# Optimization experiments

Measured on AMD Instinct MI355X. Metric: run time of the kernel, lower is better.

The kernel has to match this reference:

```python
import jax, jax.numpy as jnp
import numpy as np

N, S, A0, NPTS, L, P = 4096, 128, 5, 11, 256, 64
A = A0 + NPTS          # atoms per residue after pseudo-points
RBF_BINS = 16
RBF_MIN, RBF_MAX = 0.0, 12.0
EPS = 1e-6


def _normalize(v, axis=-1):
    return v / jnp.sqrt(jnp.sum(v * v, axis=axis, keepdims=True) + EPS)


def _extract_frames(pos):
    # pos: [N, A0, 3]; atoms 0=N, 1=CA, 2=C. Gram-Schmidt rigid frame.
    n, ca, c = pos[:, 0], pos[:, 1], pos[:, 2]
    e1 = _normalize(c - ca)
    v2 = n - ca
    u2 = v2 - e1 * jnp.sum(e1 * v2, axis=-1, keepdims=True)
    e2 = _normalize(u2)
    e3 = jnp.cross(e1, e2)
    rot = jnp.stack([e1, e2, e3], axis=-1)  # [N,3,3], columns are axes
    return rot, ca


def _distance_rbf(d):
    centers = jnp.linspace(RBF_MIN, RBF_MAX, RBF_BINS)      # [16]
    sigma = (RBF_MAX - RBF_MIN) / RBF_BINS
    z = (d[..., None] - centers) / sigma
    return jnp.exp(-z * z)


def _forward(local, pos, smol_type, smol_pos, smol_mask,
             w_points, w_type, w_local, w_dir, w_dist,
             ln_scale, ln_offset, w_mlp1, b_mlp1, w_mlp2, b_mlp2,
             w_gate, w_out):
    rot, trans = _extract_frames(pos)
    # LinearToPoints: local-frame points -> global frame
    p_local = (local @ w_points).reshape(N, NPTS, 3)
    pseudo = jnp.einsum('nij,nkj->nki', rot, p_local) + trans[:, None]
    pos_all = jnp.concatenate([pos, pseudo], axis=-2)        # [N, A, 3]

    rel = smol_pos[:, :, None, :] - pos_all[:, None, :, :]   # [N, S, A, 3]
    dist = jnp.sqrt(jnp.sum(rel * rel, axis=-1) + EPS)       # [N, S, A]
    directions = (rel / dist[..., None]).reshape(N, S, A * 3)
    distances = _distance_rbf(dist).reshape(N, S, A * RBF_BINS)

    pair = jax.nn.one_hot(smol_type, 7, dtype=local.dtype) @ w_type
    pair = pair + (local @ w_local)[:, None]
    pair = pair + directions @ w_dir
    pair = pair + distances @ w_dist                          # [N, S, P]

    mu = jnp.mean(pair, axis=-1, keepdims=True)
    var = jnp.mean((pair - mu) ** 2, axis=-1, keepdims=True)
    pair = (pair - mu) * jax.lax.rsqrt(var + 1e-5) * ln_scale + ln_offset

    pair = jax.nn.gelu(pair @ w_mlp1 + b_mlp1) @ w_mlp2 + b_mlp2

    m = smol_mask[..., None].astype(pair.dtype)
    pair = jnp.sum(pair * m, axis=1) / jnp.maximum(jnp.sum(m, axis=1), 1.0)

    gate = local @ w_gate
    pair = jax.nn.gelu(gate) * pair
    return pair @ w_out                                       # [N, L]


def setup_inputs() -> dict:
    key = jax.random.key(0)
    ks = jax.random.split(key, 16)
    sc = lambda k, sh: (jax.random.normal(k, sh, jnp.float32)
                        / np.sqrt(sh[0]).astype(np.float32))
    inp = {}
    inp['local'] = jax.random.normal(ks[0], (N, L), jnp.float32)
    inp['pos'] = jax.random.normal(ks[1], (N, A0, 3), jnp.float32) * 3.0
    inp['smol_type'] = jax.random.randint(ks[2], (N, S), 0, 7)
    inp['smol_pos'] = jax.random.normal(ks[3], (N, S, 3), jnp.float32) * 3.0
    inp['smol_mask'] = jax.random.randint(ks[4], (N, S), 0, 2).astype(bool)
    inp['w_points'] = sc(ks[5], (L, NPTS * 3))
    inp['w_type'] = sc(ks[6], (7, P))
    inp['w_local'] = sc(ks[7], (L, P))
    inp['w_dir'] = sc(ks[8], (A * 3, P))
    inp['w_dist'] = sc(ks[9], (A * RBF_BINS, P))
    inp['ln_scale'] = jnp.ones((P,), jnp.float32)
    inp['ln_offset'] = jnp.zeros((P,), jnp.float32)
    inp['w_mlp1'] = sc(ks[10], (P, 2 * P))
    inp['b_mlp1'] = jnp.zeros((2 * P,), jnp.float32)
    inp['w_mlp2'] = sc(ks[11], (2 * P, P))
    inp['b_mlp2'] = jnp.zeros((P,), jnp.float32)
    inp['w_gate'] = sc(ks[12], (L, P))
    inp['w_out'] = sc(ks[13], (P, L)) * 0.02
    return inp


def reference(local, pos, smol_type, smol_pos, smol_mask,
              w_points, w_type, w_local, w_dir, w_dist,
              ln_scale, ln_offset, w_mlp1, b_mlp1, w_mlp2, b_mlp2,
              w_gate, w_out):
    return _forward(local, pos, smol_type, smol_pos, smol_mask,
                    w_points, w_type, w_local, w_dir, w_dist,
                    ln_scale, ln_offset, w_mlp1, b_mlp1, w_mlp2, b_mlp2,
                    w_gate, w_out)
```

## Files before the change

### kernel.cpp

```cpp
#include <hip/hip_runtime.h>
#include <math.h>

#define NRES 4096
#define SS   128
#define A0C  5
#define ATOT 16
#define LD   256
#define PD   64
#define HD   128

typedef __attribute__((ext_vector_type(8))) short bf16x8;
typedef __attribute__((ext_vector_type(4))) float f32x4;
typedef __attribute__((ext_vector_type(4))) unsigned int u32x4;

__device__ __forceinline__ unsigned short f2bf(float x){
    unsigned int u = __builtin_bit_cast(unsigned int, x);
    unsigned int r = u + 0x7FFFu + ((u >> 16) & 1u);
    return (unsigned short)(r >> 16);
}
__device__ __forceinline__ unsigned short f2bfhu(float x){
    return (unsigned short)((__builtin_bit_cast(unsigned int, x) + 0x8000u) >> 16);
}
__device__ __forceinline__ unsigned int pk2bf(float lo, float hi){
    unsigned int a = __builtin_bit_cast(unsigned int, lo) + 0x8000u;
    unsigned int b = __builtin_bit_cast(unsigned int, hi) + 0x8000u;
    return __builtin_amdgcn_perm(b, a, 0x07060302u);
}
__device__ __forceinline__ float gelu_f(float x){
    float e = __builtin_amdgcn_exp2f(-2.3022082f * x * (1.0f + 0.044715f * x * x));
    return x * __builtin_amdgcn_rcpf(1.0f + e);
}
__device__ __forceinline__ f32x4 MFMA(bf16x8 a, bf16x8 b, f32x4 c){
    return __builtin_amdgcn_mfma_f32_16x16x32_bf16(a, b, c, 0, 0, 0);
}

__global__ void smol_prep(const float* __restrict__ wdist, const float* __restrict__ wdir,
                          const float* __restrict__ wm1,  const float* __restrict__ wm2,
                          unsigned short* __restrict__ ws)
{
    int i = blockIdx.x * 256 + threadIdx.x;
    if (i < 16384){
        int nn = i >> 8, k = i & 255;
        ws[i] = f2bf(wdist[k*64 + nn]);
    } else if (i < 20480){
        int j = i - 16384; int nn = j >> 6, k = j & 63;
        ws[i] = (k < 48) ? f2bf(wdir[k*64 + nn]) : (unsigned short)0;
    } else if (i < 28672){
        int j = i - 20480; int nn = j >> 6, k = j & 63;
        ws[i] = f2bf(wm1[k*128 + nn]);
    } else if (i < 36864){
        int j = i - 28672; int nn = j >> 7, k = j & 127;
        ws[i] = f2bf(wm2[k*64 + nn]);
    }
}

struct __align__(16) SMem {
    unsigned short wbuf[64*72];
    union {
        float  dist[128*17];
        unsigned short hidT[128*72];
    };
    unsigned short pairT[128*72];
    float  loc[LD];
    float  posall3[ATOT*3];
    float  pl[33];
    float  rot[9];
    float  ca3[3];
    float  wtypef[7*PD];
    float  basev[PD];
    float  gatevv[PD];
    float  lnsc[PD], lnof[PD];
    float  b1v[HD], b2v[PD];
    int    typef[SS];
    float  maskf[SS];
    float  red[4*PD];
    float  fin[PD];
    float  cnt;
};

__device__ __forceinline__ float dirv2(const SMem& sm, float px, float py, float pz,
                                       int sl, int k){
    int kc = (k < 48) ? k : 47;
    int a = (kc * 21846) >> 16;
    int c = kc - 3*a;
    float pc = (c == 0) ? px : ((c == 1) ? py : pz);
    float e = (pc - sm.posall3[a*3+c]) * __builtin_amdgcn_rcpf(sm.dist[sl*17 + a]);
    return (k < 48) ? e : 0.0f;
}

__device__ __forceinline__ void loadStage(const unsigned short* __restrict__ src, int stride,
                                          int tid, u32x4& a, u32x4& b){
    int r = tid >> 3, s = (tid & 7) * 8;
    a = *(const u32x4*)&src[r*stride + s];
    b = *(const u32x4*)&src[(r+32)*stride + s];
}
__device__ __forceinline__ void pubStage(u32x4 a, u32x4 b, unsigned short* dst, int tid){
    __syncthreads();
    int r = tid >> 3, s = (tid & 7) * 8;
    *(u32x4*)&dst[r*72 + s]      = a;
    *(u32x4*)&dst[(r+32)*72 + s] = b;
    __syncthreads();
}

#define RBF_FRAG(av, sl) do {                                               \
    float dA_ = sm.dist[(sl)*17 + 2*kk + (g>>1)] * 1.60149654f;             \
    float z0_ = dA_ - (b0c + 0.00000000f);                                  \
    float z1_ = dA_ - (b0c + 1.28119724f);                                  \
    float z2_ = dA_ - (b0c + 2.56239447f);                                  \
    float z3_ = dA_ - (b0c + 3.84359171f);                                  \
    float z4_ = dA_ - (b0c + 5.12478894f);                                  \
    float z5_ = dA_ - (b0c + 6.40598618f);                                  \
    float z6_ = dA_ - (b0c + 7.68718342f);                                  \
    float z7_ = dA_ - (b0c + 8.96838065f);                                  \
    unsigned int w0_ = pk2bf(__builtin_amdgcn_exp2f((-z0_)*z0_),            \
                             __builtin_amdgcn_exp2f((-z1_)*z1_));           \
    unsigned int w1_ = pk2bf(__builtin_amdgcn_exp2f((-z2_)*z2_),            \
                             __builtin_amdgcn_exp2f((-z3_)*z3_));           \
    unsigned int w2_ = pk2bf(__builtin_amdgcn_exp2f((-z4_)*z4_),            \
                             __builtin_amdgcn_exp2f((-z5_)*z5_));           \
    unsigned int w3_ = pk2bf(__builtin_amdgcn_exp2f((-z6_)*z6_),            \
                             __builtin_amdgcn_exp2f((-z7_)*z7_));           \
    av = __builtin_bit_cast(bf16x8, (u32x4){w0_, w1_, w2_, w3_});           \
} while(0)

__global__ __launch_bounds__(256, 3)
void smol_fused(const float* __restrict__ g_local,
                const float* __restrict__ g_pos,
                const int*   __restrict__ g_type,
                const float* __restrict__ g_spos,
                const int*   __restrict__ g_mask,
                const float* __restrict__ w_points,
                const float* __restrict__ w_local,
                const float* __restrict__ w_type,
                const float* __restrict__ ln_scale,
                const float* __restrict__ ln_offset,
                const float* __restrict__ b_mlp1,
                const float* __restrict__ b_mlp2,
                const float* __restrict__ w_gate,
                const float* __restrict__ w_out,
                const unsigned short* __restrict__ ws,
                float* __restrict__ g_out)
{
    __shared__ SMem sm;
    const int n    = blockIdx.x;
    const int tid  = threadIdx.x;
    const int wv   = tid >> 6;
    const int lane = tid & 63;
    const int cB   = lane & 15;
    const int g    = lane >> 4;
    const int sl0  = 32*wv + cB;
    const int sl1  = sl0 + 16;

    const unsigned short* wsD   = ws;
    const unsigned short* wsDir = ws + 16384;
    const unsigned short* wsM1  = ws + 20480;
    const unsigned short* wsM2  = ws + 28672;

    sm.loc[tid] = g_local[n*LD + tid];
    sm.wtypef[tid] = w_type[tid];
    if (tid < 7*PD - 256) sm.wtypef[256 + tid] = w_type[256 + tid];
    if (tid < PD){ sm.lnsc[tid] = ln_scale[tid]; sm.lnof[tid] = ln_offset[tid]; sm.b2v[tid] = b_mlp2[tid]; }
    if (tid < HD) sm.b1v[tid] = b_mlp1[tid];
    if (tid < SS){ sm.typef[tid] = g_type[n*SS + tid];
                   sm.maskf[tid] = (g_mask[n*SS + tid] != 0) ? 1.0f : 0.0f; }
    if (tid >= 128 && tid < 128 + A0C*3) sm.posall3[tid-128] = g_pos[n*A0C*3 + (tid-128)];
    __syncthreads();

    if (tid < 33){
        float a = 0.f;
        for (int i = 0; i < LD; ++i) a += sm.loc[i] * w_points[i*33 + tid];
        sm.pl[tid] = a;
    } else if (tid >= 64 && tid < 128){
        int p = tid - 64; float a = 0.f;
        for (int i = 0; i < LD; ++i) a += sm.loc[i] * w_local[i*PD + p];
        sm.basev[p] = a;
    } else if (tid >= 128 && tid < 192){
        int p = tid - 128; float a = 0.f;
        for (int i = 0; i < LD; ++i) a += sm.loc[i] * w_gate[i*PD + p];
        sm.gatevv[p] = gelu_f(a);
    } else if (tid == 255){
        float nx=sm.posall3[0], ny=sm.posall3[1], nz=sm.posall3[2];
        float cax=sm.posall3[3], cay=sm.posall3[4], caz=sm.posall3[5];
        float cx=sm.posall3[6], cy=sm.posall3[7], cz=sm.posall3[8];
        float v1x=cx-cax, v1y=cy-cay, v1z=cz-caz;
        float r = 1.0f/sqrtf(v1x*v1x + v1y*v1y + v1z*v1z + 1e-6f);
        float e1x=v1x*r, e1y=v1y*r, e1z=v1z*r;
        float v2x=nx-cax, v2y=ny-cay, v2z=nz-caz;
        float dp = e1x*v2x + e1y*v2y + e1z*v2z;
        float u2x=v2x-e1x*dp, u2y=v2y-e1y*dp, u2z=v2z-e1z*dp;
        r = 1.0f/sqrtf(u2x*u2x + u2y*u2y + u2z*u2z + 1e-6f);
        float e2x=u2x*r, e2y=u2y*r, e2z=u2z*r;
        float e3x=e1y*e2z-e1z*e2y, e3y=e1z*e2x-e1x*e2z, e3z=e1x*e2y-e1y*e2x;
        sm.rot[0]=e1x; sm.rot[1]=e2x; sm.rot[2]=e3x;
        sm.rot[3]=e1y; sm.rot[4]=e2y; sm.rot[5]=e3y;
        sm.rot[6]=e1z; sm.rot[7]=e2z; sm.rot[8]=e3z;
        sm.ca3[0]=cax; sm.ca3[1]=cay; sm.ca3[2]=caz;
    } else if (tid == 254){
        float c = 0.f;
        for (int s = 0; s < SS; ++s) c += sm.maskf[s];
        sm.cnt = c;
    }
    __syncthreads();
    if (tid < 33){
        int k = tid / 3, i2 = tid - k*3;
        sm.posall3[(A0C + k)*3 + i2] =
            sm.rot[i2*3+0]*sm.pl[k*3+0] + sm.rot[i2*3+1]*sm.pl[k*3+1] +
            sm.rot[i2*3+2]*sm.pl[k*3+2] + sm.ca3[i2];
    }
    __syncthreads();

    const float px0 = g_spos[(n*SS + sl0)*3 + 0];
    const float py0 = g_spos[(n*SS + sl0)*3 + 1];
    const float pz0 = g_spos[(n*SS + sl0)*3 + 2];
    const float px1 = g_spos[(n*SS + sl1)*3 + 0];
    const float py1 = g_spos[(n*SS + sl1)*3 + 1];
    const float pz1 = g_spos[(n*SS + sl1)*3 + 2];

    u32x4 pfa, pfb;
    loadStage(wsD, 256, tid, pfa, pfb);

    #pragma unroll
    for (int aa = 0; aa < 4; ++aa){
        int a = g*4 + aa;
        float ax = sm.posall3[a*3+0], ay = sm.posall3[a*3+1], az = sm.posall3[a*3+2];
        float rx0 = px0-ax, ry0 = py0-ay, rz0 = pz0-az;
        sm.dist[sl0*17 + a] = sqrtf(rx0*rx0 + ry0*ry0 + rz0*rz0 + 1e-6f);
        float rx1 = px1-ax, ry1 = py1-ay, rz1 = pz1-az;
        sm.dist[sl1*17 + a] = sqrtf(rx1*rx1 + ry1*ry1 + rz1*rz1 + 1e-6f);
    }

    const float lnS0 = sm.lnsc[cB+ 0], lnS1 = sm.lnsc[cB+16],
                lnS2 = sm.lnsc[cB+32], lnS3 = sm.lnsc[cB+48];
    const float lnO0 = sm.lnof[cB+ 0], lnO1 = sm.lnof[cB+16],
                lnO2 = sm.lnof[cB+32], lnO3 = sm.lnof[cB+48];
    const float bs0 = sm.basev[cB+ 0], bs1 = sm.basev[cB+16],
                bs2 = sm.basev[cB+32], bs3 = sm.basev[cB+48];
    const float b1a0 = sm.b1v[cB+0*16], b1a1 = sm.b1v[cB+1*16],
                b1a2 = sm.b1v[cB+2*16], b1a3 = sm.b1v[cB+3*16];
    const float b1b0 = sm.b1v[cB+4*16], b1b1 = sm.b1v[cB+5*16],
                b1b2 = sm.b1v[cB+6*16], b1b3 = sm.b1v[cB+7*16];

    const float b0c = (float)((g&1) * 8) * 1.28119724f;

    f32x4 accP0 = {0.f,0.f,0.f,0.f}, accP1 = accP0, accP2 = accP0, accP3 = accP0;
    f32x4 accQ0 = accP0, accQ1 = accP0, accQ2 = accP0, accQ3 = accP0;

    for (int h = 0; h < 4; ++h){
        pubStage(pfa, pfb, sm.wbuf, tid);
        if (h < 3) loadStage(wsD + (h+1)*64, 256, tid, pfa, pfb);
        else       loadStage(wsDir, 64, tid, pfa, pfb);
        #pragma unroll
        for (int kkl = 0; kkl < 2; ++kkl){
            const int kk = h*2 + kkl;
            bf16x8 av0, av1;
            RBF_FRAG(av0, sl0);
            RBF_FRAG(av1, sl1);
            const unsigned short* bb = &sm.wbuf[cB*72 + kkl*32 + g*8];
            bf16x8 B0 = *(const bf16x8*)(bb +  0*72);
            bf16x8 B1 = *(const bf16x8*)(bb + 16*72);
            bf16x8 B2 = *(const bf16x8*)(bb + 32*72);
            bf16x8 B3 = *(const bf16x8*)(bb + 48*72);
            accP0 = MFMA(av0, B0, accP0);  accQ0 = MFMA(av1, B0, accQ0);
            accP1 = MFMA(av0, B1, accP1);  accQ1 = MFMA(av1, B1, accQ1);
            accP2 = MFMA(av0, B2, accP2);  accQ2 = MFMA(av1, B2, accQ2);
            accP3 = MFMA(av0, B3, accP3);  accQ3 = MFMA(av1, B3, accQ3);
        }
    }

    pubStage(pfa, pfb, sm.wbuf, tid);
    loadStage(wsM1, 64, tid, pfa, pfb);
    #pragma unroll
    for (int kk = 0; kk < 2; ++kk){
        int k0 = kk*32 + g*8;
        unsigned int a0w0 = pk2bf(dirv2(sm,px0,py0,pz0,sl0,k0+0), dirv2(sm,px0,py0,pz0,sl0,k0+1));
        unsigned int a0w1 = pk2bf(dirv2(sm,px0,py0,pz0,sl0,k0+2), dirv2(sm,px0,py0,pz0,sl0,k0+3));
        unsigned int a0w2 = pk2bf(dirv2(sm,px0,py0,pz0,sl0,k0+4), dirv2(sm,px0,py0,pz0,sl0,k0+5));
        unsigned int a0w3 = pk2bf(dirv2(sm,px0,py0,pz0,sl0,k0+6), dirv2(sm,px0,py0,pz0,sl0,k0+7));
        bf16x8 av0 = __builtin_bit_cast(bf16x8, (u32x4){a0w0,a0w1,a0w2,a0w3});
        unsigned int a1w0 = pk2bf(dirv2(sm,px1,py1,pz1,sl1,k0+0), dirv2(sm,px1,py1,pz1,sl1,k0+1));
        unsigned int a1w1 = pk2bf(dirv2(sm,px1,py1,pz1,sl1,k0+2), dirv2(sm,px1,py1,pz1,sl1,k0+3));
        unsigned int a1w2 = pk2bf(dirv2(sm,px1,py1,pz1,sl1,k0+4), dirv2(sm,px1,py1,pz1,sl1,k0+5));
        unsigned int a1w3 = pk2bf(dirv2(sm,px1,py1,pz1,sl1,k0+6), dirv2(sm,px1,py1,pz1,sl1,k0+7));
        bf16x8 av1 = __builtin_bit_cast(bf16x8, (u32x4){a1w0,a1w1,a1w2,a1w3});
        const unsigned short* bb = &sm.wbuf[cB*72 + k0];
        bf16x8 B0 = *(const bf16x8*)(bb +  0*72);
        bf16x8 B1 = *(const bf16x8*)(bb + 16*72);
        bf16x8 B2 = *(const bf16x8*)(bb + 32*72);
        bf16x8 B3 = *(const bf16x8*)(bb + 48*72);
        accP0 = MFMA(av0, B0, accP0);  accQ0 = MFMA(av1, B0, accQ0);
        accP1 = MFMA(av0, B1, accP1);  accQ1 = MFMA(av1, B1, accQ1);
        accP2 = MFMA(av0, B2, accP2);  accQ2 = MFMA(av1, B2, accQ2);
        accP3 = MFMA(av0, B3, accP3);  accQ3 = MFMA(av1, B3, accQ3);
    }

    #pragma unroll
    for (int t = 0; t < 2; ++t){
        #pragma unroll
        for (int r = 0; r < 4; ++r){
            int slr = 32*wv + 16*t + g*4 + r;
            int ty  = sm.typef[slr];
            float a0 = (t==0 ? accP0[r] : accQ0[r]);
            float a1 = (t==0 ? accP1[r] : accQ1[r]);
            float a2 = (t==0 ? accP2[r] : accQ2[r]);
            float a3 = (t==0 ? accP3[r] : accQ3[r]);
            float v0 = a0 + bs0 + sm.wtypef[ty*PD + cB +  0];
            float v1 = a1 + bs1 + sm.wtypef[ty*PD + cB + 16];
            float v2 = a2 + bs2 + sm.wtypef[ty*PD + cB + 32];
            float v3 = a3 + bs3 + sm.wtypef[ty*PD + cB + 48];
            float ssum = v0+v1+v2+v3;
            ssum += __shfl_xor(ssum,1); ssum += __shfl_xor(ssum,2);
            ssum += __shfl_xor(ssum,4); ssum += __shfl_xor(ssum,8);
            float mu = ssum * (1.0f/64.0f);
            float d0=v0-mu, d1=v1-mu, d2=v2-mu, d3=v3-mu;
            float sq = d0*d0+d1*d1+d2*d2+d3*d3;
            sq += __shfl_xor(sq,1); sq += __shfl_xor(sq,2);
            sq += __shfl_xor(sq,4); sq += __shfl_xor(sq,8);
            float inv = __builtin_amdgcn_rsqf(sq*(1.0f/64.0f) + 1e-5f);
            unsigned short* pr = &sm.pairT[slr*72];
            pr[cB +  0] = f2bfhu(d0*inv*lnS0 + lnO0);
            pr[cB + 16] = f2bfhu(d1*inv*lnS1 + lnO1);
            pr[cB + 32] = f2bfhu(d2*inv*lnS2 + lnO2);
            pr[cB + 48] = f2bfhu(d3*inv*lnS3 + lnO3);
        }
    }

    f32x4 accO0 = {0.f,0.f,0.f,0.f}, accO1 = accO0, accO2 = accO0, accO3 = accO0;
    f32x4 accN0 = accO0, accN1 = accO0, accN2 = accO0, accN3 = accO0;

    f32x4 accH0 = {0.f,0.f,0.f,0.f}, accH1 = accH0, accH2 = accH0, accH3 = accH0;
    f32x4 accI0 = accH0, accI1 = accH0, accI2 = accH0, accI3 = accH0;
    pubStage(pfa, pfb, sm.wbuf, tid);
    loadStage(wsM2, 128, tid, pfa, pfb);
    #pragma unroll
    for (int kk = 0; kk < 2; ++kk){
        bf16x8 a0 = *(const bf16x8*)&sm.pairT[sl0*72 + kk*32 + g*8];
        bf16x8 a1 = *(const bf16x8*)&sm.pairT[sl1*72 + kk*32 + g*8];
        const unsigned short* bb = &sm.wbuf[cB*72 + kk*32 + g*8];
        bf16x8 B0 = *(const bf16x8*)(bb + 0*16*72);
        bf16x8 B1 = *(const bf16x8*)(bb + 1*16*72);
        bf16x8 B2 = *(const bf16x8*)(bb + 2*16*72);
        bf16x8 B3 = *(const bf16x8*)(bb + 3*16*72);
        accH0 = MFMA(a0, B0, accH0);  accI0 = MFMA(a1, B0, accI0);
        accH1 = MFMA(a0, B1, accH1);  accI1 = MFMA(a1, B1, accI1);
        accH2 = MFMA(a0, B2, accH2);  accI2 = MFMA(a1, B2, accI2);
        accH3 = MFMA(a0, B3, accH3);  accI3 = MFMA(a1, B3, accI3);
    }
    #pragma unroll
    for (int r = 0; r < 4; ++r){
        int slr0 = 32*wv + g*4 + r;
        unsigned short* hr0 = &sm.hidT[slr0*72];
        hr0[cB + 0*16] = f2bfhu(gelu_f(accH0[r] + b1a0));
        hr0[cB + 1*16] = f2bfhu(gelu_f(accH1[r] + b1a1));
        hr0[cB + 2*16] = f2bfhu(gelu_f(accH2[r] + b1a2));
        hr0[cB + 3*16] = f2bfhu(gelu_f(accH3[r] + b1a3));
        unsigned short* hr1 = &sm.hidT[(slr0+16)*72];
        hr1[cB + 0*16] = f2bfhu(gelu_f(accI0[r] + b1a0));
        hr1[cB + 1*16] = f2bfhu(gelu_f(accI1[r] + b1a1));
        hr1[cB + 2*16] = f2bfhu(gelu_f(accI2[r] + b1a2));
        hr1[cB + 3*16] = f2bfhu(gelu_f(accI3[r] + b1a3));
    }

    pubStage(pfa, pfb, sm.wbuf, tid);
    loadStage(wsM1 + 64*64, 64, tid, pfa, pfb);
    #pragma unroll
    for (int kkl = 0; kkl < 2; ++kkl){
        bf16x8 a0 = *(const bf16x8*)&sm.hidT[sl0*72 + kkl*32 + g*8];
        bf16x8 a1 = *(const bf16x8*)&sm.hidT[sl1*72 + kkl*32 + g*8];
        const unsigned short* bb = &sm.wbuf[cB*72 + kkl*32 + g*8];
        bf16x8 B0 = *(const bf16x8*)(bb + 0*16*72);
        bf16x8 B1 = *(const bf16x8*)(bb + 1*16*72);
        bf16x8 B2 = *(const bf16x8*)(bb + 2*16*72);
        bf16x8 B3 = *(const bf16x8*)(bb + 3*16*72);
        accO0 = MFMA(a0, B0, accO0);  accN0 = MFMA(a1, B0, accN0);
        accO1 = MFMA(a0, B1, accO1);  accN1 = MFMA(a1, B1, accN1);
        accO2 = MFMA(a0, B2, accO2);  accN2 = MFMA(a1, B2, accN2);
        accO3 = MFMA(a0, B3, accO3);  accN3 = MFMA(a1, B3, accN3);
    }

    f32x4 accH4 = {0.f,0.f,0.f,0.f}, accH5 = accH4, accH6 = accH4, accH7 = accH4;
    f32x4 accI4 = accH4, accI5 = accH4, accI6 = accH4, accI7 = accH4;
    pubStage(pfa, pfb, sm.wbuf, tid);
    loadStage(wsM2 + 64, 128, tid, pfa, pfb);
    #pragma unroll
    for (int kk = 0; kk < 2; ++kk){
        bf16x8 a0 = *(const bf16x8*)&sm.pairT[sl0*72 + kk*32 + g*8];
        bf16x8 a1 = *(const bf16x8*)&sm.pairT[sl1*72 + kk*32 + g*8];
        const unsigned short* bb = &sm.wbuf[cB*72 + kk*32 + g*8];
        bf16x8 B0 = *(const bf16x8*)(bb + 0*16*72);
        bf16x8 B1 = *(const bf16x8*)(bb + 1*16*72);
        bf16x8 B2 = *(const bf16x8*)(bb + 2*16*72);
        bf16x8 B3 = *(const bf16x8*)(bb + 3*16*72);
        accH4 = MFMA(a0, B0, accH4);  accI4 = MFMA(a1, B0, accI4);
        accH5 = MFMA(a0, B1, accH5);  accI5 = MFMA(a1, B1, accI5);
        accH6 = MFMA(a0, B2, accH6);  accI6 = MFMA(a1, B2, accI6);
        accH7 = MFMA(a0, B3, accH7);  accI7 = MFMA(a1, B3, accI7);
    }
    #pragma unroll
    for (int r = 0; r < 4; ++r){
        int slr0 = 32*wv + g*4 + r;
        unsigned short* hr0 = &sm.hidT[slr0*72];
        hr0[cB + 0*16] = f2bfhu(gelu_f(accH4[r] + b1b0));
        hr0[cB + 1*16] = f2bfhu(gelu_f(accH5[r] + b1b1));
        hr0[cB + 2*16] = f2bfhu(gelu_f(accH6[r] + b1b2));
        hr0[cB + 3*16] = f2bfhu(gelu_f(accH7[r] + b1b3));
        unsigned short* hr1 = &sm.hidT[(slr0+16)*72];
        hr1[cB + 0*16] = f2bfhu(gelu_f(accI4[r] + b1b0));
        hr1[cB + 1*16] = f2bfhu(gelu_f(accI5[r] + b1b1));
        hr1[cB + 2*16] = f2bfhu(gelu_f(accI6[r] + b1b2));
        hr1[cB + 3*16] = f2bfhu(gelu_f(accI7[r] + b1b3));
    }

    pubStage(pfa, pfb, sm.wbuf, tid);
    #pragma unroll
    for (int kkl = 0; kkl < 2; ++kkl){
        bf16x8 a0 = *(const bf16x8*)&sm.hidT[sl0*72 + kkl*32 + g*8];
        bf16x8 a1 = *(const bf16x8*)&sm.hidT[sl1*72 + kkl*32 + g*8];
        const unsigned short* bb = &sm.wbuf[cB*72 + kkl*32 + g*8];
        bf16x8 B0 = *(const bf16x8*)(bb + 0*16*72);
        bf16x8 B1 = *(const bf16x8*)(bb + 1*16*72);
        bf16x8 B2 = *(const bf16x8*)(bb + 2*16*72);
        bf16x8 B3 = *(const bf16x8*)(bb + 3*16*72);
        accO0 = MFMA(a0, B0, accO0);  accN0 = MFMA(a1, B0, accN0);
        accO1 = MFMA(a0, B1, accO1);  accN1 = MFMA(a1, B1, accN1);
        accO2 = MFMA(a0, B2, accO2);  accN2 = MFMA(a1, B2, accN2);
        accO3 = MFMA(a0, B3, accO3);  accN3 = MFMA(a1, B3, accN3);
    }

    float pooled0 = 0.f, pooled1 = 0.f, pooled2 = 0.f, pooled3 = 0.f;
    #pragma unroll
    for (int r = 0; r < 4; ++r){
        float m0f = sm.maskf[32*wv + g*4 + r];
        float m1f = sm.maskf[32*wv + 16 + g*4 + r];
        pooled0 += m0f * accO0[r] + m1f * accN0[r];
        pooled1 += m0f * accO1[r] + m1f * accN1[r];
        pooled2 += m0f * accO2[r] + m1f * accN2[r];
        pooled3 += m0f * accO3[r] + m1f * accN3[r];
    }

    pooled0 += __shfl_xor(pooled0,16); pooled0 += __shfl_xor(pooled0,32);
    pooled1 += __shfl_xor(pooled1,16); pooled1 += __shfl_xor(pooled1,32);
    pooled2 += __shfl_xor(pooled2,16); pooled2 += __shfl_xor(pooled2,32);
    pooled3 += __shfl_xor(pooled3,16); pooled3 += __shfl_xor(pooled3,32);
    if (g == 0){
        sm.red[wv*PD + cB +  0] = pooled0;
        sm.red[wv*PD + cB + 16] = pooled1;
        sm.red[wv*PD + cB + 32] = pooled2;
        sm.red[wv*PD + cB + 48] = pooled3;
    }
    __syncthreads();
    if (tid < PD){
        float v = sm.red[tid] + sm.red[PD + tid] + sm.red[2*PD + tid] + sm.red[3*PD + tid];
        float mc = fmaxf(sm.cnt, 1.0f);
        v = (v + sm.cnt * sm.b2v[tid]) / mc;
        sm.fin[tid] = sm.gatevv[tid] * v;
    }
    __syncthreads();
    {
        float a = 0.f;
        #pragma unroll 4
        for (int p = 0; p < PD; ++p) a += sm.fin[p] * w_out[p*LD + tid];
        g_out[n*LD + tid] = a;
    }
}

extern "C" void kernel_launch(void* const* d_in, const int* in_sizes, int n_in,
                              void* d_out, int out_size, void* d_ws, size_t ws_size,
                              hipStream_t stream)
{
    (void)in_sizes; (void)n_in; (void)out_size; (void)ws_size;
    const float* g_local   = (const float*)d_in[0];
    const float* g_pos     = (const float*)d_in[1];
    const int*   g_type    = (const int*)  d_in[2];
    const float* g_spos    = (const float*)d_in[3];
    const int*   g_mask    = (const int*)  d_in[4];
    const float* w_points  = (const float*)d_in[5];
    const float* w_type    = (const float*)d_in[6];
    const float* w_local   = (const float*)d_in[7];
    const float* w_dir     = (const float*)d_in[8];
    const float* w_dist    = (const float*)d_in[9];
    const float* ln_scale  = (const float*)d_in[10];
    const float* ln_offset = (const float*)d_in[11];
    const float* w_mlp1    = (const float*)d_in[12];
    const float* b_mlp1    = (const float*)d_in[13];
    const float* w_mlp2    = (const float*)d_in[14];
    const float* b_mlp2    = (const float*)d_in[15];
    const float* w_gate    = (const float*)d_in[16];
    const float* w_out     = (const float*)d_in[17];

    unsigned short* ws = (unsigned short*)d_ws;

    smol_prep<<<dim3(144), dim3(256), 0, stream>>>(w_dist, w_dir, w_mlp1, w_mlp2, ws);

    smol_fused<<<dim3(NRES), dim3(256), 0, stream>>>(
        g_local, g_pos, g_type, g_spos, g_mask,
        w_points, w_local, w_type, ln_scale, ln_offset,
        b_mlp1, b_mlp2, w_gate, w_out, ws, (float*)d_out);
}
```

Before: 132.6 us.

## Keep layer-normed pair tile in registers via transposed MFMA and shuffles

Measured after the change: 122.3 us. -7.8%, faster.

```diff
diff --git a/kernel.cpp b/kernel.cpp
--- a/kernel.cpp
+++ b/kernel.cpp
@@ -60,21 +60,21 @@
         float  dist[128*17];
         unsigned short hidT[128*72];
     };
-    unsigned short pairT[128*72];
     float  loc[LD];
     float  posall3[ATOT*3];
+    float  wtypef[7*PD];
+    float  basev[PD];
+    float  lnsc[PD], lnof[PD];
+    float  b1v[HD];
+    float  b2v[PD];
+    float  gatevv[PD];
+    float  maskf[SS];
+    float  red[4*PD];
+    float  fin[PD];
+    int    typef[SS];
     float  pl[33];
     float  rot[9];
     float  ca3[3];
-    float  wtypef[7*PD];
-    float  basev[PD];
-    float  gatevv[PD];
-    float  lnsc[PD], lnof[PD];
-    float  b1v[HD], b2v[PD];
-    int    typef[SS];
-    float  maskf[SS];
-    float  red[4*PD];
-    float  fin[PD];
     float  cnt;
 };
 
@@ -123,7 +123,44 @@
     av = __builtin_bit_cast(bf16x8, (u32x4){w0_, w1_, w2_, w3_});           \
 } while(0)
 
-__global__ __launch_bounds__(256, 3)
+#define MK_FRAG(F, Lm0, Lm1) do {                                           \
+    float a0_ = __shfl(Lm0[0], srcA), b0_ = __shfl(Lm1[0], srcA);           \
+    float a1_ = __shfl(Lm0[1], srcA), b1_ = __shfl(Lm1[1], srcA);           \
+    float a2_ = __shfl(Lm0[2], srcA), b2_ = __shfl(Lm1[2], srcA);           \
+    float a3_ = __shfl(Lm0[3], srcA), b3_ = __shfl(Lm1[3], srcA);           \
+    float a4_ = __shfl(Lm0[0], srcB), b4_ = __shfl(Lm1[0], srcB);           \
+    float a5_ = __shfl(Lm0[1], srcB), b5_ = __shfl(Lm1[1], srcB);           \
+    float a6_ = __shfl(Lm0[2], srcB), b6_ = __shfl(Lm1[2], srcB);           \
+    float a7_ = __shfl(Lm0[3], srcB), b7_ = __shfl(Lm1[3], srcB);           \
+    float v0_ = hi ? b0_ : a0_;  float v1_ = hi ? b1_ : a1_;                \
+    float v2_ = hi ? b2_ : a2_;  float v3_ = hi ? b3_ : a3_;                \
+    float v4_ = hi ? b4_ : a4_;  float v5_ = hi ? b5_ : a5_;                \
+    float v6_ = hi ? b6_ : a6_;  float v7_ = hi ? b7_ : a7_;                \
+    F = __builtin_bit_cast(bf16x8, (u32x4){pk2bf(v0_,v1_), pk2bf(v2_,v3_),  \
+                                           pk2bf(v4_,v5_), pk2bf(v6_,v7_)});\
+} while(0)
+
+#define TILE_LN(L0, L1, L2, L3, A0, A1, A2, A3, tyv) do {                   \
+    f32x4 v0_ = A0 + bV0 + *(const f32x4*)&sm.wtypef[(tyv)*PD + pb +  0];   \
+    f32x4 v1_ = A1 + bV1 + *(const f32x4*)&sm.wtypef[(tyv)*PD + pb + 16];   \
+    f32x4 v2_ = A2 + bV2 + *(const f32x4*)&sm.wtypef[(tyv)*PD + pb + 32];   \
+    f32x4 v3_ = A3 + bV3 + *(const f32x4*)&sm.wtypef[(tyv)*PD + pb + 48];   \
+    float ss_ = v0_[0]+v0_[1]+v0_[2]+v0_[3] + v1_[0]+v1_[1]+v1_[2]+v1_[3]   \
+              + v2_[0]+v2_[1]+v2_[2]+v2_[3] + v3_[0]+v3_[1]+v3_[2]+v3_[3];  \
+    ss_ += __shfl_xor(ss_,16); ss_ += __shfl_xor(ss_,32);                   \
+    float mu_ = ss_ * (1.0f/64.0f);                                         \
+    f32x4 d0_ = v0_ - mu_, d1_ = v1_ - mu_, d2_ = v2_ - mu_, d3_ = v3_ - mu_;\
+    float sq_ = d0_[0]*d0_[0]+d0_[1]*d0_[1]+d0_[2]*d0_[2]+d0_[3]*d0_[3]     \
+              + d1_[0]*d1_[0]+d1_[1]*d1_[1]+d1_[2]*d1_[2]+d1_[3]*d1_[3]     \
+              + d2_[0]*d2_[0]+d2_[1]*d2_[1]+d2_[2]*d2_[2]+d2_[3]*d2_[3]     \
+              + d3_[0]*d3_[0]+d3_[1]*d3_[1]+d3_[2]*d3_[2]+d3_[3]*d3_[3];    \
+    sq_ += __shfl_xor(sq_,16); sq_ += __shfl_xor(sq_,32);                   \
+    float inv_ = __builtin_amdgcn_rsqf(sq_*(1.0f/64.0f) + 1e-5f);           \
+    L0 = d0_*inv_*sV0 + oV0;  L1 = d1_*inv_*sV1 + oV1;                      \
+    L2 = d2_*inv_*sV2 + oV2;  L3 = d3_*inv_*sV3 + oV3;                      \
+} while(0)
+
+__global__ __launch_bounds__(256, 4)
 void smol_fused(const float* __restrict__ g_local,
                 const float* __restrict__ g_pos,
                 const int*   __restrict__ g_type,
@@ -229,18 +266,11 @@
         sm.dist[sl1*17 + a] = sqrtf(rx1*rx1 + ry1*ry1 + rz1*rz1 + 1e-6f);
     }
 
-    const float lnS0 = sm.lnsc[cB+ 0], lnS1 = sm.lnsc[cB+16],
-                lnS2 = sm.lnsc[cB+32], lnS3 = sm.lnsc[cB+48];
-    const float lnO0 = sm.lnof[cB+ 0], lnO1 = sm.lnof[cB+16],
-                lnO2 = sm.lnof[cB+32], lnO3 = sm.lnof[cB+48];
-    const float bs0 = sm.basev[cB+ 0], bs1 = sm.basev[cB+16],
-                bs2 = sm.basev[cB+32], bs3 = sm.basev[cB+48];
+    const float b0c = (float)((g&1) * 8) * 1.28119724f;
     const float b1a0 = sm.b1v[cB+0*16], b1a1 = sm.b1v[cB+1*16],
                 b1a2 = sm.b1v[cB+2*16], b1a3 = sm.b1v[cB+3*16];
     const float b1b0 = sm.b1v[cB+4*16], b1b1 = sm.b1v[cB+5*16],
                 b1b2 = sm.b1v[cB+6*16], b1b3 = sm.b1v[cB+7*16];
-
-    const float b0c = (float)((g&1) * 8) * 1.28119724f;
 
     f32x4 accP0 = {0.f,0.f,0.f,0.f}, accP1 = accP0, accP2 = accP0, accP3 = accP0;
     f32x4 accQ0 = accP0, accQ1 = accP0, accQ2 = accP0, accQ3 = accP0;
@@ -260,10 +290,10 @@
             bf16x8 B1 = *(const bf16x8*)(bb + 16*72);
             bf16x8 B2 = *(const bf16x8*)(bb + 32*72);
             bf16x8 B3 = *(const bf16x8*)(bb + 48*72);
-            accP0 = MFMA(av0, B0, accP0);  accQ0 = MFMA(av1, B0, accQ0);
-            accP1 = MFMA(av0, B1, accP1);  accQ1 = MFMA(av1, B1, accQ1);
-            accP2 = MFMA(av0, B2, accP2);  accQ2 = MFMA(av1, B2, accQ2);
-            accP3 = MFMA(av0, B3, accP3);  accQ3 = MFMA(av1, B3, accQ3);
+            accP0 = MFMA(B0, av0, accP0);  accQ0 = MFMA(B0, av1, accQ0);
+            accP1 = MFMA(B1, av0, accP1);  accQ1 = MFMA(B1, av1, accQ1);
+            accP2 = MFMA(B2, av0, accP2);  accQ2 = MFMA(B2, av1, accQ2);
+            accP3 = MFMA(B3, av0, accP3);  accQ3 = MFMA(B3, av1, accQ3);
         }
     }
 
@@ -287,41 +317,44 @@
         bf16x8 B1 = *(const bf16x8*)(bb + 16*72);
         bf16x8 B2 = *(const bf16x8*)(bb + 32*72);
         bf16x8 B3 = *(const bf16x8*)(bb + 48*72);
-        accP0 = MFMA(av0, B0, accP0);  accQ0 = MFMA(av1, B0, accQ0);
-        accP1 = MFMA(av0, B1, accP1);  accQ1 = MFMA(av1, B1, accQ1);
-        accP2 = MFMA(av0, B2, accP2);  accQ2 = MFMA(av1, B2, accQ2);
-        accP3 = MFMA(av0, B3, accP3);  accQ3 = MFMA(av1, B3, accQ3);
-    }
-
-    #pragma unroll
-    for (int t = 0; t < 2; ++t){
-        #pragma unroll
-        for (int r = 0; r < 4; ++r){
-            int slr = 32*wv + 16*t + g*4 + r;
-            int ty  = sm.typef[slr];
-            float a0 = (t==0 ? accP0[r] : accQ0[r]);
-            float a1 = (t==0 ? accP1[r] : accQ1[r]);
-            float a2 = (t==0 ? accP2[r] : accQ2[r]);
-            float a3 = (t==0 ? accP3[r] : accQ3[r]);
-            float v0 = a0 + bs0 + sm.wtypef[ty*PD + cB +  0];
-            float v1 = a1 + bs1 + sm.wtypef[ty*PD + cB + 16];
-            float v2 = a2 + bs2 + sm.wtypef[ty*PD + cB + 32];
-            float v3 = a3 + bs3 + sm.wtypef[ty*PD + cB + 48];
-            float ssum = v0+v1+v2+v3;
-            ssum += __shfl_xor(ssum,1); ssum += __shfl_xor(ssum,2);
-            ssum += __shfl_xor(ssum,4); ssum += __shfl_xor(ssum,8);
-            float mu = ssum * (1.0f/64.0f);
-            float d0=v0-mu, d1=v1-mu, d2=v2-mu, d3=v3-mu;
-            float sq = d0*d0+d1*d1+d2*d2+d3*d3;
-            sq += __shfl_xor(sq,1); sq += __shfl_xor(sq,2);
-            sq += __shfl_xor(sq,4); sq += __shfl_xor(sq,8);
-            float inv = __builtin_amdgcn_rsqf(sq*(1.0f/64.0f) + 1e-5f);
-            unsigned short* pr = &sm.pairT[slr*72];
-            pr[cB +  0] = f2bfhu(d0*inv*lnS0 + lnO0);
-            pr[cB + 16] = f2bfhu(d1*inv*lnS1 + lnO1);
-            pr[cB + 32] = f2bfhu(d2*inv*lnS2 + lnO2);
-            pr[cB + 48] = f2bfhu(d3*inv*lnS3 + lnO3);
-        }
+        accP0 = MFMA(B0, av0, accP0);  accQ0 = MFMA(B0, av1, accQ0);
+        accP1 = MFMA(B1, av0, accP1);  accQ1 = MFMA(B1, av1, accQ1);
+        accP2 = MFMA(B2, av0, accP2);  accQ2 = MFMA(B2, av1, accQ2);
+        accP3 = MFMA(B3, av0, accP3);  accQ3 = MFMA(B3, av1, accQ3);
+    }
+
+    const int pb  = 4*g;
+    const bool hi = (g >> 1);
+    const int srcA = ((g&1) << 5) + cB;
+    const int srcB = srcA + 16;
+
+    const f32x4 bV0 = *(const f32x4*)&sm.basev[pb +  0];
+    const f32x4 bV1 = *(const f32x4*)&sm.basev[pb + 16];
+    const f32x4 bV2 = *(const f32x4*)&sm.basev[pb + 32];
+    const f32x4 bV3 = *(const f32x4*)&sm.basev[pb + 48];
+    const f32x4 sV0 = *(const f32x4*)&sm.lnsc[pb +  0];
+    const f32x4 sV1 = *(const f32x4*)&sm.lnsc[pb + 16];
+    const f32x4 sV2 = *(const f32x4*)&sm.lnsc[pb + 32];
+    const f32x4 sV3 = *(const f32x4*)&sm.lnsc[pb + 48];
+    const f32x4 oV0 = *(const f32x4*)&sm.lnof[pb +  0];
+    const f32x4 oV1 = *(const f32x4*)&sm.lnof[pb + 16];
+    const f32x4 oV2 = *(const f32x4*)&sm.lnof[pb + 32];
+    const f32x4 oV3 = *(const f32x4*)&sm.lnof[pb + 48];
+
+    bf16x8 F00, F01, F10, F11;
+    {
+        int ty0 = sm.typef[sl0];
+        f32x4 L0, L1, L2, L3;
+        TILE_LN(L0, L1, L2, L3, accP0, accP1, accP2, accP3, ty0);
+        MK_FRAG(F00, L0, L1);
+        MK_FRAG(F01, L2, L3);
+    }
+    {
+        int ty1 = sm.typef[sl1];
+        f32x4 L0, L1, L2, L3;
+        TILE_LN(L0, L1, L2, L3, accQ0, accQ1, accQ2, accQ3, ty1);
+        MK_FRAG(F10, L0, L1);
+        MK_FRAG(F11, L2, L3);
     }
 
     f32x4 accO0 = {0.f,0.f,0.f,0.f}, accO1 = accO0, accO2 = accO0, accO3 = accO0;
@@ -333,8 +366,8 @@
     loadStage(wsM2, 128, tid, pfa, pfb);
     #pragma unroll
     for (int kk = 0; kk < 2; ++kk){
-        bf16x8 a0 = *(const bf16x8*)&sm.pairT[sl0*72 + kk*32 + g*8];
-        bf16x8 a1 = *(const bf16x8*)&sm.pairT[sl1*72 + kk*32 + g*8];
+        bf16x8 a0 = kk ? F01 : F00;
+        bf16x8 a1 = kk ? F11 : F10;
         const unsigned short* bb = &sm.wbuf[cB*72 + kk*32 + g*8];
         bf16x8 B0 = *(const bf16x8*)(bb + 0*16*72);
         bf16x8 B1 = *(const bf16x8*)(bb + 1*16*72);
@@ -383,8 +416,8 @@
     loadStage(wsM2 + 64, 128, tid, pfa, pfb);
     #pragma unroll
     for (int kk = 0; kk < 2; ++kk){
-        bf16x8 a0 = *(const bf16x8*)&sm.pairT[sl0*72 + kk*32 + g*8];
-        bf16x8 a1 = *(const bf16x8*)&sm.pairT[sl1*72 + kk*32 + g*8];
+        bf16x8 a0 = kk ? F01 : F00;
+        bf16x8 a1 = kk ? F11 : F10;
         const unsigned short* bb = &sm.wbuf[cB*72 + kk*32 + g*8];
         bf16x8 B0 = *(const bf16x8*)(bb + 0*16*72);
         bf16x8 B1 = *(const bf16x8*)(bb + 1*16*72);
```
